# Optimization experiments

Measured on AMD Instinct MI355X. Metric: run time of the kernel, lower is better.

The kernel has to match this reference:

```python
import jax, jax.numpy as jnp
import numpy as np

ARAP_WEIGHT = 1.0


def _decoder(code, W1, b1, W2, b2, W3, b3):
    # code: [D] -> vertices [N, 3]
    h = jax.nn.relu(code @ W1 + b1)
    h = jax.nn.relu(h @ W2 + b2)
    v = h @ W3 + b3
    return v.reshape(-1, 3)


def _arap_per_vertex(xyz1, recon, nbr, num_nbr, wmat):
    # xyz1, recon: [N,3]; nbr: [N,K] int; num_nbr: [N]; wmat: [N,K]
    N, K = nbr.shape
    mask = (jnp.arange(K)[None, :] < num_nbr[:, None]).astype(wmat.dtype)
    w = wmat * mask                              # zero out padded neighbors
    e_rest = xyz1[nbr] - xyz1[:, None, :]        # [N,K,3] rest-pose edges (gather)
    e_def = recon[nbr] - recon[:, None, :]       # [N,K,3] deformed edges (gather)
    # weighted covariance per vertex: S_i = sum_k w_ik e_ik e'_ik^T  -> [N,3,3]
    S = jnp.einsum('nk,nka,nkb->nab', w, e_rest, e_def)
    U, _, Vt = jnp.linalg.svd(S)
    V = jnp.swapaxes(Vt, -1, -2)
    R0 = jnp.einsum('nab,ncb->nac', V, U)        # V U^T
    d = jnp.linalg.det(R0)                       # reflection fix
    diag = jnp.stack([jnp.ones_like(d), jnp.ones_like(d), d], axis=-1)  # [N,3]
    R = jnp.einsum('nab,nb,ncb->nac', V, diag, U)
    R = jax.lax.stop_gradient(R)                 # local-global: rotations fixed in bwd
    e_rot = jnp.einsum('nab,nkb->nka', R, e_rest)
    resid = e_def - e_rot
    return jnp.sum(w * jnp.sum(resid * resid, axis=-1), axis=-1)  # [N]


def setup_inputs() -> dict:
    key = jax.random.key(0)
    ks = jax.random.split(key, 12)
    N, K, D = 20000, 16, 256
    H1, H2 = 512, 1024
    inp = {
        'code': jax.random.normal(ks[0], (D,), jnp.float32),
        'xyz1': jax.random.normal(ks[1], (N, 3), jnp.float32),
        'weightMatrix': jax.random.uniform(ks[2], (N, K), jnp.float32),
        'W1': jax.random.normal(ks[3], (D, H1), jnp.float32) * (1.0 / np.sqrt(D)),
        'b1': jax.random.normal(ks[4], (H1,), jnp.float32) * 0.01,
        'W2': jax.random.normal(ks[5], (H1, H2), jnp.float32) * (1.0 / np.sqrt(H1)),
        'b2': jax.random.normal(ks[6], (H2,), jnp.float32) * 0.01,
        'W3': jax.random.normal(ks[7], (H2, N * 3), jnp.float32) * (1.0 / np.sqrt(H2)),
        'b3': jax.random.normal(ks[8], (N * 3,), jnp.float32) * 0.01,
        'neighborsMatrix': jax.random.randint(ks[9], (N, K), 0, N, jnp.int64),
        'numNeighbors': jax.random.randint(ks[10], (N,), 0, 17, jnp.int64),
    }
    return inp


def reference(code, xyz1, weightMatrix, W1, b1, W2, b2, W3, b3,
              neighborsMatrix, numNeighbors):
    def energy(c):
        recon = _decoder(c, W1, b1, W2, b2, W3, b3)
        pv = _arap_per_vertex(xyz1, recon, neighborsMatrix, numNeighbors, weightMatrix)
        return ARAP_WEIGHT * jnp.mean(pv)

    E, g = jax.value_and_grad(energy)(code)
    # torch module returns (arapEnergy.item(), -code.grad) with arapEnergy = -E
    return (-E, g)
```

## Files before the change

kernel.cpp:

```cpp
#include <hip/hip_runtime.h>
#include <hip/hip_bf16.h>

#define N_V   20000
#define KNB   16
#define DCODE 256
#define H1    512
#define H2    1024
#define M3    60000

#define OFF_L1P   0
#define OFF_L2P   4096
#define OFF_VPART 12288
#define OFF_V     492288
#define OFF_GV    552288
#define OFF_GZ2   612288
#define OFF_GZ1   613312
#define OFF_H1    613824
#define OFF_H2    614336
#define OFF_HC    615360
#define OFF_LIST  616384
#define OFF_CNT   617408
#define OFF_E     617410


__global__ void k_l1p(const float* __restrict__ code, const float* __restrict__ W1,
                      float* __restrict__ ws) {
    int m = blockIdx.x * 256 + threadIdx.x;
    int d0 = blockIdx.y * 32;
    float acc = 0.f;
#pragma unroll
    for (int d = 0; d < 32; ++d)
        acc += code[d0 + d] * W1[(size_t)(d0 + d) * H1 + m];
    ws[OFF_L1P + blockIdx.y * H1 + m] = acc;
    int gid = (blockIdx.y * 2 + blockIdx.x) * 256 + threadIdx.x;
    for (int idx = gid; idx < M3; idx += 4096) ws[OFF_GV + idx] = 0.f;
    if (gid == 0) { ws[OFF_E] = 0.f; ws[OFF_E + 1] = 0.f; }
}

__global__ void k_l2p(const float* __restrict__ b1, const float* __restrict__ W2,
                      float* __restrict__ ws) {
    __shared__ float h1s[64];
    int dz = blockIdx.y, d0 = dz * 64;
    int t = threadIdx.x;
    if (t < 64) {
        float s = b1[d0 + t];
#pragma unroll
        for (int p = 0; p < 8; ++p) s += ws[OFF_L1P + p * H1 + d0 + t];
        float h = fmaxf(s, 0.f);
        h1s[t] = h;
        if (blockIdx.x == 0) ws[OFF_H1 + d0 + t] = h;
    }
    __syncthreads();
    int m = blockIdx.x * 256 + t;
    float acc = 0.f;
#pragma unroll 8
    for (int d = 0; d < 64; ++d)
        acc += h1s[d] * W2[(size_t)(d0 + d) * H2 + m];
    ws[OFF_L2P + dz * H2 + m] = acc;
}

__global__ void k_compact(const float* __restrict__ b2, float* __restrict__ ws) {
    __shared__ int scan[256];
    int t = threadIdx.x;
    float h[4]; int c = 0;
#pragma unroll
    for (int q = 0; q < 4; ++q) {
        int j = t * 4 + q;
        float s = b2[j];
#pragma unroll
        for (int p = 0; p < 8; ++p) s += ws[OFF_L2P + p * H2 + j];
        float hv = fmaxf(s, 0.f);
        ws[OFF_H2 + j] = hv;
        h[q] = hv;
        c += (hv > 0.f) ? 1 : 0;
    }
    scan[t] = c;
    __syncthreads();
    for (int off = 1; off < 256; off <<= 1) {
        int x = (t >= off) ? scan[t - off] : 0;
        __syncthreads();
        scan[t] += x;
        __syncthreads();
    }
    int base = scan[t] - c;
    int* list = reinterpret_cast<int*>(&ws[OFF_LIST]);
#pragma unroll
    for (int q = 0; q < 4; ++q) {
        if (h[q] > 0.f) {
            list[base] = t * 4 + q;
            ws[OFF_HC + base] = h[q];
            ++base;
        }
    }
    if (t == 255) *reinterpret_cast<int*>(&ws[OFF_CNT]) = scan[255];
}

__global__ void k_l3p(const float* __restrict__ W3, float* __restrict__ ws) {
    __shared__ int   rlist[128];
    __shared__ float rh[128];
    int jz = blockIdx.y;
    int cnt = *reinterpret_cast<const int*>(&ws[OFF_CNT]);
    int per = (cnt + 7) >> 3;
    int s0 = jz * per;
    int s1 = s0 + per; if (s1 > cnt) s1 = cnt;
    int n = s1 - s0;
    int t = threadIdx.x;
    if (t < 128 && t < n) {
        rlist[t] = reinterpret_cast<const int*>(&ws[OFF_LIST])[s0 + t];
        rh[t]    = ws[OFF_HC + s0 + t];
    }
    __syncthreads();
    int m4 = blockIdx.x * 1024 + t * 4;
    if (m4 >= M3) return;
    float ax = 0.f, ay = 0.f, az = 0.f, aw = 0.f;
    int ii = 0;
    for (; ii + 3 < n; ii += 4) {
        int r0 = rlist[ii], r1 = rlist[ii + 1], r2 = rlist[ii + 2], r3 = rlist[ii + 3];
        float h0 = rh[ii], h1v = rh[ii + 1], h2v = rh[ii + 2], h3 = rh[ii + 3];
        float4 w0 = *reinterpret_cast<const float4*>(&W3[(size_t)r0 * M3 + m4]);
        float4 w1 = *reinterpret_cast<const float4*>(&W3[(size_t)r1 * M3 + m4]);
        float4 w2 = *reinterpret_cast<const float4*>(&W3[(size_t)r2 * M3 + m4]);
        float4 w3 = *reinterpret_cast<const float4*>(&W3[(size_t)r3 * M3 + m4]);
        ax += h0 * w0.x + h1v * w1.x + h2v * w2.x + h3 * w3.x;
        ay += h0 * w0.y + h1v * w1.y + h2v * w2.y + h3 * w3.y;
        az += h0 * w0.z + h1v * w1.z + h2v * w2.z + h3 * w3.z;
        aw += h0 * w0.w + h1v * w1.w + h2v * w2.w + h3 * w3.w;
    }
    for (; ii < n; ++ii) {
        int r0 = rlist[ii]; float h0 = rh[ii];
        float4 w0 = *reinterpret_cast<const float4*>(&W3[(size_t)r0 * M3 + m4]);
        ax += h0 * w0.x; ay += h0 * w0.y; az += h0 * w0.z; aw += h0 * w0.w;
    }
    float4 acc = make_float4(ax, ay, az, aw);
    *reinterpret_cast<float4*>(&ws[OFF_VPART + jz * M3 + m4]) = acc;
}

__global__ void k_vred(const float* __restrict__ b3, float* __restrict__ ws) {
    int i4 = blockIdx.x * 256 + threadIdx.x;
    if (i4 < M3 / 4) {
        int m = i4 * 4;
        float4 a = *reinterpret_cast<const float4*>(&b3[m]);
#pragma unroll
        for (int jz = 0; jz < 8; ++jz) {
            float4 p = *reinterpret_cast<const float4*>(&ws[OFF_VPART + jz * M3 + m]);
            a.x += p.x; a.y += p.y; a.z += p.z; a.w += p.w;
        }
        *reinterpret_cast<float4*>(&ws[OFF_V + m]) = a;
    }
}


__device__ inline void jrot(double a[3][3], double v[3][3], int p, int q) {
    double apq = a[p][q];
    if (fabs(apq) < 1e-300) return;
    double theta = (a[q][q] - a[p][p]) / (2.0 * apq);
    double t;
    if (fabs(theta) > 1.0e100) t = 0.5 / theta;
    else t = copysign(1.0, theta) / (fabs(theta) + sqrt(theta * theta + 1.0));
    double c = 1.0 / sqrt(t * t + 1.0);
    double s = t * c;
    double app = a[p][p], aqq = a[q][q];
    a[p][p] = app - t * apq;
    a[q][q] = aqq + t * apq;
    a[p][q] = 0.0; a[q][p] = 0.0;
    int r = 3 - p - q;
    double arp = a[r][p], arq = a[r][q];
    a[r][p] = c * arp - s * arq; a[p][r] = a[r][p];
    a[r][q] = s * arp + c * arq; a[q][r] = a[r][q];
#pragma unroll
    for (int k2 = 0; k2 < 3; ++k2) {
        double vkp = v[k2][p], vkq = v[k2][q];
        v[k2][p] = c * vkp - s * vkq;
        v[k2][q] = s * vkp + c * vkq;
    }
}

__device__ void compute_R(const double S[3][3], double R[3][3]) {
    double A[3][3], V[3][3];
#pragma unroll
    for (int a = 0; a < 3; ++a)
#pragma unroll
        for (int b = 0; b < 3; ++b) {
            double s = 0.0;
#pragma unroll
            for (int c = 0; c < 3; ++c) s += S[c][a] * S[c][b];
            A[a][b] = s;
            V[a][b] = (a == b) ? 1.0 : 0.0;
        }
    for (int sweep = 0; sweep < 20; ++sweep) {
        double off = A[0][1]*A[0][1] + A[0][2]*A[0][2] + A[1][2]*A[1][2];
        double dg  = A[0][0]*A[0][0] + A[1][1]*A[1][1] + A[2][2]*A[2][2];
        if (off <= 1e-28 * (dg + 1e-300)) break;
        jrot(A, V, 0, 1); jrot(A, V, 0, 2); jrot(A, V, 1, 2);
    }
    int id[3] = {0, 1, 2};
    if (A[id[0]][id[0]] < A[id[1]][id[1]]) { int t = id[0]; id[0] = id[1]; id[1] = t; }
    if (A[id[0]][id[0]] < A[id[2]][id[2]]) { int t = id[0]; id[0] = id[2]; id[2] = t; }
    if (A[id[1]][id[1]] < A[id[2]][id[2]]) { int t = id[1]; id[1] = id[2]; id[2] = t; }
    double v0[3], v1[3], v2[3];
#pragma unroll
    for (int r = 0; r < 3; ++r) {
        v0[r] = V[r][id[0]]; v1[r] = V[r][id[1]]; v2[r] = V[r][id[2]];
    }
    double u0[3], u1[3], u2[3];
#pragma unroll
    for (int a = 0; a < 3; ++a)
        u0[a] = S[a][0]*v0[0] + S[a][1]*v0[1] + S[a][2]*v0[2];
    double n0 = sqrt(u0[0]*u0[0] + u0[1]*u0[1] + u0[2]*u0[2]);
    if (!(n0 > 1e-150)) {
#pragma unroll
        for (int a = 0; a < 3; ++a)
#pragma unroll
            for (int c = 0; c < 3; ++c) R[a][c] = (a == c) ? 1.0 : 0.0;
        return;
    }
#pragma unroll
    for (int a = 0; a < 3; ++a) u0[a] /= n0;
    double t1[3];
#pragma unroll
    for (int a = 0; a < 3; ++a)
        t1[a] = S[a][0]*v1[0] + S[a][1]*v1[1] + S[a][2]*v1[2];
    double dp = u0[0]*t1[0] + u0[1]*t1[1] + u0[2]*t1[2];
#pragma unroll
    for (int a = 0; a < 3; ++a) t1[a] -= dp * u0[a];
    double n1 = sqrt(t1[0]*t1[0] + t1[1]*t1[1] + t1[2]*t1[2]);
    if (n1 > 1e-9 * n0) {
#pragma unroll
        for (int a = 0; a < 3; ++a) u1[a] = t1[a] / n1;
    } else {
        int m = (fabs(u0[0]) <= fabs(u0[1]) && fabs(u0[0]) <= fabs(u0[2])) ? 0
              : (fabs(u0[1]) <= fabs(u0[2]) ? 1 : 2);
        double e[3] = {0.0, 0.0, 0.0}; e[m] = 1.0;
        double cx[3] = { u0[1]*e[2] - u0[2]*e[1],
                         u0[2]*e[0] - u0[0]*e[2],
                         u0[0]*e[1] - u0[1]*e[0] };
        double nn = sqrt(cx[0]*cx[0] + cx[1]*cx[1] + cx[2]*cx[2]);
#pragma unroll
        for (int a = 0; a < 3; ++a) u1[a] = cx[a] / nn;
    }
    u2[0] = u0[1]*u1[2] - u0[2]*u1[1];
    u2[1] = u0[2]*u1[0] - u0[0]*u1[2];
    u2[2] = u0[0]*u1[1] - u0[1]*u1[0];
    double d = v0[0]*(v1[1]*v2[2] - v1[2]*v2[1])
             - v0[1]*(v1[0]*v2[2] - v1[2]*v2[0])
             + v0[2]*(v1[0]*v2[1] - v1[1]*v2[0]);
#pragma unroll
    for (int a = 0; a < 3; ++a)
#pragma unroll
        for (int c = 0; c < 3; ++c)
            R[a][c] = v0[a]*u0[c] + v1[a]*u1[c] + d * (v2[a]*u2[c]);
}

__global__ void k_arap(const float* __restrict__ xyz1, const float* __restrict__ wmat,
                       const int* __restrict__ nbr, const int* __restrict__ nnum,
                       float* __restrict__ ws) {
    const float* recon = ws + OFF_V;
    float* gv = ws + OFF_GV;
    int i = blockIdx.x * 256 + threadIdx.x;
    double pv = 0.0;
    if (i < N_V) {
        int num = nnum[i];
        if (num > KNB) num = KNB;
        double cr0 = xyz1[3*i], cr1 = xyz1[3*i+1], cr2 = xyz1[3*i+2];
        double cd0 = recon[3*i], cd1 = recon[3*i+1], cd2 = recon[3*i+2];
        double S[3][3] = {{0,0,0},{0,0,0},{0,0,0}};
        for (int k = 0; k < num; ++k) {
            int j = nbr[i*KNB + k];
            double w = wmat[i*KNB + k];
            double er[3] = { xyz1[3*j] - cr0, xyz1[3*j+1] - cr1, xyz1[3*j+2] - cr2 };
            double ed[3] = { recon[3*j] - cd0, recon[3*j+1] - cd1, recon[3*j+2] - cd2 };
#pragma unroll
            for (int a = 0; a < 3; ++a)
#pragma unroll
                for (int b = 0; b < 3; ++b) S[a][b] += w * er[a] * ed[b];
        }
        double R[3][3];
        compute_R(S, R);
        const float gscale = 2.0f / (float)N_V;
        for (int k = 0; k < num; ++k) {
            int j = nbr[i*KNB + k];
            double w = wmat[i*KNB + k];
            double er[3] = { xyz1[3*j] - cr0, xyz1[3*j+1] - cr1, xyz1[3*j+2] - cr2 };
            double ed[3] = { recon[3*j] - cd0, recon[3*j+1] - cd1, recon[3*j+2] - cd2 };
            double rr0 = R[0][0]*er[0] + R[0][1]*er[1] + R[0][2]*er[2];
            double rr1 = R[1][0]*er[0] + R[1][1]*er[1] + R[1][2]*er[2];
            double rr2 = R[2][0]*er[0] + R[2][1]*er[1] + R[2][2]*er[2];
            double r0 = ed[0] - rr0, r1 = ed[1] - rr1, r2 = ed[2] - rr2;
            pv += w * (r0*r0 + r1*r1 + r2*r2);
            float g0 = gscale * (float)(w * r0);
            float g1 = gscale * (float)(w * r1);
            float g2 = gscale * (float)(w * r2);
            atomicAdd(&gv[3*j+0],  g0);
            atomicAdd(&gv[3*j+1],  g1);
            atomicAdd(&gv[3*j+2],  g2);
            atomicAdd(&gv[3*i+0], -g0);
            atomicAdd(&gv[3*i+1], -g1);
            atomicAdd(&gv[3*i+2], -g2);
        }
    }
    __shared__ double red[256];
    red[threadIdx.x] = pv;
    __syncthreads();
    for (int s = 128; s > 0; s >>= 1) {
        if (threadIdx.x < s) red[threadIdx.x] += red[threadIdx.x + s];
        __syncthreads();
    }
    if (threadIdx.x == 0)
        atomicAdd(reinterpret_cast<double*>(ws + OFF_E), red[0]);
}


__global__ void k_gh2(const float* __restrict__ W3, float* __restrict__ ws) {
    int j = blockIdx.x;
    float* gz2 = ws + OFF_GZ2;
    float h2v = ws[OFF_H2 + j];
    if (h2v <= 0.f) {
        if (threadIdx.x == 0) gz2[j] = 0.f;
        return;
    }
    const float4* w3r = reinterpret_cast<const float4*>(W3 + (size_t)j * M3);
    const float4* gv4 = reinterpret_cast<const float4*>(ws + OFF_GV);
    float acc = 0.f;
    for (int it = threadIdx.x; it < M3 / 4; it += 256) {
        float4 a = w3r[it], b = gv4[it];
        acc += a.x*b.x + a.y*b.y + a.z*b.z + a.w*b.w;
    }
    for (int m = 32; m; m >>= 1) acc += __shfl_xor(acc, m);
    __shared__ float wsum[4];
    if ((threadIdx.x & 63) == 0) wsum[threadIdx.x >> 6] = acc;
    __syncthreads();
    if (threadIdx.x == 0) gz2[j] = wsum[0] + wsum[1] + wsum[2] + wsum[3];
}

__global__ void k_gh1(const float* __restrict__ W2, float* __restrict__ ws) {
    int wv = threadIdx.x >> 6, ln = threadIdx.x & 63;
    int i = blockIdx.x * 4 + wv;
    const float* gz2 = ws + OFF_GZ2;
    float acc = 0.f;
#pragma unroll
    for (int it = 0; it < H2 / 64; ++it) {
        int jj = ln + it * 64;
        acc += W2[(size_t)i * H2 + jj] * gz2[jj];
    }
    for (int m = 32; m; m >>= 1) acc += __shfl_xor(acc, m);
    if (ln == 0) ws[OFF_GZ1 + i] = (ws[OFF_H1 + i] > 0.f) ? acc : 0.f;
}

__global__ void k_gcode(const float* __restrict__ W1, float* __restrict__ ws,
                        float* __restrict__ out) {
    int wv = threadIdx.x >> 6, ln = threadIdx.x & 63;
    int d = blockIdx.x * 4 + wv;
    const float* gz1 = ws + OFF_GZ1;
    float acc = 0.f;
#pragma unroll
    for (int it = 0; it < H1 / 64; ++it) {
        int ii = ln + it * 64;
        acc += W1[(size_t)d * H1 + ii] * gz1[ii];
    }
    for (int m = 32; m; m >>= 1) acc += __shfl_xor(acc, m);
    if (ln == 0) out[1 + d] = acc;
    if (blockIdx.x == 0 && threadIdx.x == 0) {
        double E = *reinterpret_cast<const double*>(ws + OFF_E);
        out[0] = (float)(-(E / (double)N_V));
    }
}

extern "C" void kernel_launch(void* const* d_in, const int* in_sizes, int n_in,
                              void* d_out, int out_size, void* d_ws, size_t ws_size,
                              hipStream_t stream) {
    const float* code = (const float*)d_in[0];
    const float* xyz1 = (const float*)d_in[1];
    const float* wmat = (const float*)d_in[2];
    const float* W1   = (const float*)d_in[3];
    const float* b1   = (const float*)d_in[4];
    const float* W2   = (const float*)d_in[5];
    const float* b2   = (const float*)d_in[6];
    const float* W3   = (const float*)d_in[7];
    const float* b3   = (const float*)d_in[8];
    const int*   nbr  = (const int*)d_in[9];
    const int*   nnum = (const int*)d_in[10];
    float* out = (float*)d_out;
    float* ws  = (float*)d_ws;

    k_l1p    <<<dim3(2, 8),  256, 0, stream>>>(code, W1, ws);
    k_l2p    <<<dim3(4, 8),  256, 0, stream>>>(b1, W2, ws);
    k_compact<<<1,           256, 0, stream>>>(b2, ws);
    k_l3p    <<<dim3(59, 8), 256, 0, stream>>>(W3, ws);
    k_vred   <<<59,          256, 0, stream>>>(b3, ws);
    k_arap   <<<79,          256, 0, stream>>>(xyz1, wmat, nbr, nnum, ws);
    k_gh2    <<<1024,        256, 0, stream>>>(W3, ws);
    k_gh1    <<<128,         256, 0, stream>>>(W2, ws);
    k_gcode  <<<64,          256, 0, stream>>>(W1, ws, out);
}
```

Before: 117.5 us.

## Split ARAP into float32 rotation and gradient kernels with smaller blocks

New measurement: 120.9 us. 1.03x slower.

```diff
diff --git a/kernel.cpp b/kernel.cpp
--- a/kernel.cpp
+++ b/kernel.cpp
@@ -21,6 +21,7 @@
 #define OFF_LIST  616384
 #define OFF_CNT   617408
 #define OFF_E     617410
+#define OFF_R     617412
 
 
 __global__ void k_l1p(const float* __restrict__ code, const float* __restrict__ W1,
@@ -71,6 +72,7 @@
         for (int p = 0; p < 8; ++p) s += ws[OFF_L2P + p * H2 + j];
         float hv = fmaxf(s, 0.f);
         ws[OFF_H2 + j] = hv;
+        ws[OFF_GZ2 + j] = 0.f;
         h[q] = hv;
         c += (hv > 0.f) ? 1 : 0;
     }
@@ -150,100 +152,100 @@
 }
 
 
-__device__ inline void jrot(double a[3][3], double v[3][3], int p, int q) {
-    double apq = a[p][q];
-    if (fabs(apq) < 1e-300) return;
-    double theta = (a[q][q] - a[p][p]) / (2.0 * apq);
-    double t;
-    if (fabs(theta) > 1.0e100) t = 0.5 / theta;
-    else t = copysign(1.0, theta) / (fabs(theta) + sqrt(theta * theta + 1.0));
-    double c = 1.0 / sqrt(t * t + 1.0);
-    double s = t * c;
-    double app = a[p][p], aqq = a[q][q];
+__device__ inline void jrotf(float a[3][3], float v[3][3], int p, int q) {
+    float apq = a[p][q];
+    if (fabsf(apq) < 1e-30f) return;
+    float theta = (a[q][q] - a[p][p]) / (2.0f * apq);
+    float t;
+    if (fabsf(theta) > 1e18f) t = 0.5f / theta;
+    else t = copysignf(1.0f, theta) / (fabsf(theta) + sqrtf(theta * theta + 1.0f));
+    float c = 1.0f / sqrtf(t * t + 1.0f);
+    float s = t * c;
+    float app = a[p][p], aqq = a[q][q];
     a[p][p] = app - t * apq;
     a[q][q] = aqq + t * apq;
-    a[p][q] = 0.0; a[q][p] = 0.0;
+    a[p][q] = 0.0f; a[q][p] = 0.0f;
     int r = 3 - p - q;
-    double arp = a[r][p], arq = a[r][q];
+    float arp = a[r][p], arq = a[r][q];
     a[r][p] = c * arp - s * arq; a[p][r] = a[r][p];
     a[r][q] = s * arp + c * arq; a[q][r] = a[r][q];
 #pragma unroll
     for (int k2 = 0; k2 < 3; ++k2) {
-        double vkp = v[k2][p], vkq = v[k2][q];
+        float vkp = v[k2][p], vkq = v[k2][q];
         v[k2][p] = c * vkp - s * vkq;
         v[k2][q] = s * vkp + c * vkq;
     }
 }
 
-__device__ void compute_R(const double S[3][3], double R[3][3]) {
-    double A[3][3], V[3][3];
+__device__ void compute_Rf(const float S[3][3], float R[3][3]) {
+    float A[3][3], V[3][3];
 #pragma unroll
     for (int a = 0; a < 3; ++a)
 #pragma unroll
         for (int b = 0; b < 3; ++b) {
-            double s = 0.0;
+            float s = 0.0f;
 #pragma unroll
             for (int c = 0; c < 3; ++c) s += S[c][a] * S[c][b];
             A[a][b] = s;
-            V[a][b] = (a == b) ? 1.0 : 0.0;
+            V[a][b] = (a == b) ? 1.0f : 0.0f;
         }
-    for (int sweep = 0; sweep < 20; ++sweep) {
-        double off = A[0][1]*A[0][1] + A[0][2]*A[0][2] + A[1][2]*A[1][2];
-        double dg  = A[0][0]*A[0][0] + A[1][1]*A[1][1] + A[2][2]*A[2][2];
-        if (off <= 1e-28 * (dg + 1e-300)) break;
-        jrot(A, V, 0, 1); jrot(A, V, 0, 2); jrot(A, V, 1, 2);
+    for (int sweep = 0; sweep < 15; ++sweep) {
+        float off = A[0][1]*A[0][1] + A[0][2]*A[0][2] + A[1][2]*A[1][2];
+        float dg  = A[0][0]*A[0][0] + A[1][1]*A[1][1] + A[2][2]*A[2][2];
+        if (off <= 1e-12f * (dg + 1e-30f)) break;
+        jrotf(A, V, 0, 1); jrotf(A, V, 0, 2); jrotf(A, V, 1, 2);
     }
     int id[3] = {0, 1, 2};
     if (A[id[0]][id[0]] < A[id[1]][id[1]]) { int t = id[0]; id[0] = id[1]; id[1] = t; }
     if (A[id[0]][id[0]] < A[id[2]][id[2]]) { int t = id[0]; id[0] = id[2]; id[2] = t; }
     if (A[id[1]][id[1]] < A[id[2]][id[2]]) { int t = id[1]; id[1] = id[2]; id[2] = t; }
-    double v0[3], v1[3], v2[3];
+    float v0[3], v1[3], v2[3];
 #pragma unroll
     for (int r = 0; r < 3; ++r) {
         v0[r] = V[r][id[0]]; v1[r] = V[r][id[1]]; v2[r] = V[r][id[2]];
     }
-    double u0[3], u1[3], u2[3];
+    float u0[3], u1[3], u2[3];
 #pragma unroll
     for (int a = 0; a < 3; ++a)
         u0[a] = S[a][0]*v0[0] + S[a][1]*v0[1] + S[a][2]*v0[2];
-    double n0 = sqrt(u0[0]*u0[0] + u0[1]*u0[1] + u0[2]*u0[2]);
-    if (!(n0 > 1e-150)) {
+    float n0 = sqrtf(u0[0]*u0[0] + u0[1]*u0[1] + u0[2]*u0[2]);
+    if (!(n0 > 1e-20f)) {
 #pragma unroll
         for (int a = 0; a < 3; ++a)
 #pragma unroll
-            for (int c = 0; c < 3; ++c) R[a][c] = (a == c) ? 1.0 : 0.0;
+            for (int c = 0; c < 3; ++c) R[a][c] = (a == c) ? 1.0f : 0.0f;
         return;
     }
 #pragma unroll
     for (int a = 0; a < 3; ++a) u0[a] /= n0;
-    double t1[3];
+    float t1[3];
 #pragma unroll
     for (int a = 0; a < 3; ++a)
         t1[a] = S[a][0]*v1[0] + S[a][1]*v1[1] + S[a][2]*v1[2];
-    double dp = u0[0]*t1[0] + u0[1]*t1[1] + u0[2]*t1[2];
+    float dp = u0[0]*t1[0] + u0[1]*t1[1] + u0[2]*t1[2];
 #pragma unroll
     for (int a = 0; a < 3; ++a) t1[a] -= dp * u0[a];
-    double n1 = sqrt(t1[0]*t1[0] + t1[1]*t1[1] + t1[2]*t1[2]);
-    if (n1 > 1e-9 * n0) {
+    float n1 = sqrtf(t1[0]*t1[0] + t1[1]*t1[1] + t1[2]*t1[2]);
+    if (n1 > 1e-5f * n0) {
 #pragma unroll
         for (int a = 0; a < 3; ++a) u1[a] = t1[a] / n1;
     } else {
-        int m = (fabs(u0[0]) <= fabs(u0[1]) && fabs(u0[0]) <= fabs(u0[2])) ? 0
-              : (fabs(u0[1]) <= fabs(u0[2]) ? 1 : 2);
-        double e[3] = {0.0, 0.0, 0.0}; e[m] = 1.0;
-        double cx[3] = { u0[1]*e[2] - u0[2]*e[1],
-                         u0[2]*e[0] - u0[0]*e[2],
-                         u0[0]*e[1] - u0[1]*e[0] };
-        double nn = sqrt(cx[0]*cx[0] + cx[1]*cx[1] + cx[2]*cx[2]);
+        int m = (fabsf(u0[0]) <= fabsf(u0[1]) && fabsf(u0[0]) <= fabsf(u0[2])) ? 0
+              : (fabsf(u0[1]) <= fabsf(u0[2]) ? 1 : 2);
+        float e[3] = {0.0f, 0.0f, 0.0f}; e[m] = 1.0f;
+        float cx[3] = { u0[1]*e[2] - u0[2]*e[1],
+                        u0[2]*e[0] - u0[0]*e[2],
+                        u0[0]*e[1] - u0[1]*e[0] };
+        float nn = sqrtf(cx[0]*cx[0] + cx[1]*cx[1] + cx[2]*cx[2]);
 #pragma unroll
         for (int a = 0; a < 3; ++a) u1[a] = cx[a] / nn;
     }
     u2[0] = u0[1]*u1[2] - u0[2]*u1[1];
     u2[1] = u0[2]*u1[0] - u0[0]*u1[2];
     u2[2] = u0[0]*u1[1] - u0[1]*u1[0];
-    double d = v0[0]*(v1[1]*v2[2] - v1[2]*v2[1])
-             - v0[1]*(v1[0]*v2[2] - v1[2]*v2[0])
-             + v0[2]*(v1[0]*v2[1] - v1[1]*v2[0]);
+    float d = v0[0]*(v1[1]*v2[2] - v1[2]*v2[1])
+            - v0[1]*(v1[0]*v2[2] - v1[2]*v2[0])
+            + v0[2]*(v1[0]*v2[1] - v1[1]*v2[0]);
 #pragma unroll
     for (int a = 0; a < 3; ++a)
 #pragma unroll
@@ -251,85 +253,97 @@
             R[a][c] = v0[a]*u0[c] + v1[a]*u1[c] + d * (v2[a]*u2[c]);
 }
 
-__global__ void k_arap(const float* __restrict__ xyz1, const float* __restrict__ wmat,
-                       const int* __restrict__ nbr, const int* __restrict__ nnum,
-                       float* __restrict__ ws) {
+__global__ void k_arapR(const float* __restrict__ xyz1, const float* __restrict__ wmat,
+                        const int* __restrict__ nbr, const int* __restrict__ nnum,
+                        float* __restrict__ ws) {
+    int i = blockIdx.x * 64 + threadIdx.x;
+    if (i >= N_V) return;
+    const float* recon = ws + OFF_V;
+    int num = nnum[i]; if (num > KNB) num = KNB;
+    float cr0 = xyz1[3*i], cr1 = xyz1[3*i+1], cr2 = xyz1[3*i+2];
+    float cd0 = recon[3*i], cd1 = recon[3*i+1], cd2 = recon[3*i+2];
+    float S[3][3] = {{0,0,0},{0,0,0},{0,0,0}};
+    for (int k = 0; k < num; ++k) {
+        int j = nbr[i*KNB + k];
+        float w = wmat[i*KNB + k];
+        float er0 = xyz1[3*j]   - cr0, er1 = xyz1[3*j+1] - cr1, er2 = xyz1[3*j+2] - cr2;
+        float ed0 = recon[3*j]  - cd0, ed1 = recon[3*j+1] - cd1, ed2 = recon[3*j+2] - cd2;
+        S[0][0] += w*er0*ed0; S[0][1] += w*er0*ed1; S[0][2] += w*er0*ed2;
+        S[1][0] += w*er1*ed0; S[1][1] += w*er1*ed1; S[1][2] += w*er1*ed2;
+        S[2][0] += w*er2*ed0; S[2][1] += w*er2*ed1; S[2][2] += w*er2*ed2;
+    }
+    float R[3][3];
+    compute_Rf(S, R);
+#pragma unroll
+    for (int a = 0; a < 3; ++a)
+#pragma unroll
+        for (int c = 0; c < 3; ++c)
+            ws[OFF_R + (a*3 + c) * N_V + i] = R[a][c];
+}
+
+__global__ void k_arapG(const float* __restrict__ xyz1, const float* __restrict__ wmat,
+                        const int* __restrict__ nbr, const int* __restrict__ nnum,
+                        float* __restrict__ ws) {
     const float* recon = ws + OFF_V;
     float* gv = ws + OFF_GV;
-    int i = blockIdx.x * 256 + threadIdx.x;
+    int i = blockIdx.x * 64 + threadIdx.x;
     double pv = 0.0;
     if (i < N_V) {
-        int num = nnum[i];
-        if (num > KNB) num = KNB;
-        double cr0 = xyz1[3*i], cr1 = xyz1[3*i+1], cr2 = xyz1[3*i+2];
-        double cd0 = recon[3*i], cd1 = recon[3*i+1], cd2 = recon[3*i+2];
-        double S[3][3] = {{0,0,0},{0,0,0},{0,0,0}};
+        int num = nnum[i]; if (num > KNB) num = KNB;
+        float cr0 = xyz1[3*i], cr1 = xyz1[3*i+1], cr2 = xyz1[3*i+2];
+        float cd0 = recon[3*i], cd1 = recon[3*i+1], cd2 = recon[3*i+2];
+        float R00 = ws[OFF_R + 0*N_V + i], R01 = ws[OFF_R + 1*N_V + i], R02 = ws[OFF_R + 2*N_V + i];
+        float R10 = ws[OFF_R + 3*N_V + i], R11 = ws[OFF_R + 4*N_V + i], R12 = ws[OFF_R + 5*N_V + i];
+        float R20 = ws[OFF_R + 6*N_V + i], R21 = ws[OFF_R + 7*N_V + i], R22 = ws[OFF_R + 8*N_V + i];
+        const float gscale = 2.0f / (float)N_V;
+        float own0 = 0.f, own1 = 0.f, own2 = 0.f;
         for (int k = 0; k < num; ++k) {
             int j = nbr[i*KNB + k];
-            double w = wmat[i*KNB + k];
-            double er[3] = { xyz1[3*j] - cr0, xyz1[3*j+1] - cr1, xyz1[3*j+2] - cr2 };
-            double ed[3] = { recon[3*j] - cd0, recon[3*j+1] - cd1, recon[3*j+2] - cd2 };
-#pragma unroll
-            for (int a = 0; a < 3; ++a)
-#pragma unroll
-                for (int b = 0; b < 3; ++b) S[a][b] += w * er[a] * ed[b];
+            float w = wmat[i*KNB + k];
+            float er0 = xyz1[3*j]   - cr0, er1 = xyz1[3*j+1] - cr1, er2 = xyz1[3*j+2] - cr2;
+            float ed0 = recon[3*j]  - cd0, ed1 = recon[3*j+1] - cd1, ed2 = recon[3*j+2] - cd2;
+            float r0 = ed0 - (R00*er0 + R01*er1 + R02*er2);
+            float r1 = ed1 - (R10*er0 + R11*er1 + R12*er2);
+            float r2 = ed2 - (R20*er0 + R21*er1 + R22*er2);
+            pv += (double)(w * (r0*r0 + r1*r1 + r2*r2));
+            float g0 = gscale * w * r0;
+            float g1 = gscale * w * r1;
+            float g2 = gscale * w * r2;
+            atomicAdd(&gv[3*j+0], g0);
+            atomicAdd(&gv[3*j+1], g1);
+            atomicAdd(&gv[3*j+2], g2);
+            own0 += g0; own1 += g1; own2 += g2;
         }
-        double R[3][3];
-        compute_R(S, R);
-        const float gscale = 2.0f / (float)N_V;
-        for (int k = 0; k < num; ++k) {
-            int j = nbr[i*KNB + k];
-            double w = wmat[i*KNB + k];
-            double er[3] = { xyz1[3*j] - cr0, xyz1[3*j+1] - cr1, xyz1[3*j+2] - cr2 };
-            double ed[3] = { recon[3*j] - cd0, recon[3*j+1] - cd1, recon[3*j+2] - cd2 };
-            double rr0 = R[0][0]*er[0] + R[0][1]*er[1] + R[0][2]*er[2];
-            double rr1 = R[1][0]*er[0] + R[1][1]*er[1] + R[1][2]*er[2];
-            double rr2 = R[2][0]*er[0] + R[2][1]*er[1] + R[2][2]*er[2];
-            double r0 = ed[0] - rr0, r1 = ed[1] - rr1, r2 = ed[2] - rr2;
-            pv += w * (r0*r0 + r1*r1 + r2*r2);
-            float g0 = gscale * (float)(w * r0);
-            float g1 = gscale * (float)(w * r1);
-            float g2 = gscale * (float)(w * r2);
-            atomicAdd(&gv[3*j+0],  g0);
-            atomicAdd(&gv[3*j+1],  g1);
-            atomicAdd(&gv[3*j+2],  g2);
-            atomicAdd(&gv[3*i+0], -g0);
-            atomicAdd(&gv[3*i+1], -g1);
-            atomicAdd(&gv[3*i+2], -g2);
+        if (num > 0) {
+            atomicAdd(&gv[3*i+0], -own0);
+            atomicAdd(&gv[3*i+1], -own1);
+            atomicAdd(&gv[3*i+2], -own2);
         }
     }
-    __shared__ double red[256];
-    red[threadIdx.x] = pv;
-    __syncthreads();
-    for (int s = 128; s > 0; s >>= 1) {
-        if (threadIdx.x < s) red[threadIdx.x] += red[threadIdx.x + s];
-        __syncthreads();
-    }
+#pragma unroll
+    for (int m = 32; m; m >>= 1) pv += __shfl_xor(pv, m);
     if (threadIdx.x == 0)
-        atomicAdd(reinterpret_cast<double*>(ws + OFF_E), red[0]);
+        atomicAdd(reinterpret_cast<double*>(ws + OFF_E), pv);
 }
 
 
 __global__ void k_gh2(const float* __restrict__ W3, float* __restrict__ ws) {
-    int j = blockIdx.x;
-    float* gz2 = ws + OFF_GZ2;
-    float h2v = ws[OFF_H2 + j];
-    if (h2v <= 0.f) {
-        if (threadIdx.x == 0) gz2[j] = 0.f;
-        return;
-    }
+    int b = blockIdx.x;
+    int cnt = *reinterpret_cast<const int*>(&ws[OFF_CNT]);
+    if (b >= cnt) return;
+    int j = reinterpret_cast<const int*>(&ws[OFF_LIST])[b];
     const float4* w3r = reinterpret_cast<const float4*>(W3 + (size_t)j * M3);
     const float4* gv4 = reinterpret_cast<const float4*>(ws + OFF_GV);
     float acc = 0.f;
     for (int it = threadIdx.x; it < M3 / 4; it += 256) {
-        float4 a = w3r[it], b = gv4[it];
-        acc += a.x*b.x + a.y*b.y + a.z*b.z + a.w*b.w;
+        float4 a = w3r[it], g = gv4[it];
+        acc += a.x*g.x + a.y*g.y + a.z*g.z + a.w*g.w;
     }
     for (int m = 32; m; m >>= 1) acc += __shfl_xor(acc, m);
     __shared__ float wsum[4];
     if ((threadIdx.x & 63) == 0) wsum[threadIdx.x >> 6] = acc;
     __syncthreads();
-    if (threadIdx.x == 0) gz2[j] = wsum[0] + wsum[1] + wsum[2] + wsum[3];
+    if (threadIdx.x == 0) ws[OFF_GZ2 + j] = wsum[0] + wsum[1] + wsum[2] + wsum[3];
 }
 
 __global__ void k_gh1(const float* __restrict__ W2, float* __restrict__ ws) {
@@ -387,7 +401,8 @@
     k_compact<<<1,           256, 0, stream>>>(b2, ws);
     k_l3p    <<<dim3(59, 8), 256, 0, stream>>>(W3, ws);
     k_vred   <<<59,          256, 0, stream>>>(b3, ws);
-    k_arap   <<<79,          256, 0, stream>>>(xyz1, wmat, nbr, nnum, ws);
+    k_arapR  <<<313,          64, 0, stream>>>(xyz1, wmat, nbr, nnum, ws);
+    k_arapG  <<<313,          64, 0, stream>>>(xyz1, wmat, nbr, nnum, ws);
     k_gh2    <<<1024,        256, 0, stream>>>(W3, ws);
     k_gh1    <<<128,         256, 0, stream>>>(W2, ws);
     k_gcode  <<<64,          256, 0, stream>>>(W1, ws, out);
```
